# Performance work log

Measured on AMD Instinct MI355X. Metric: run time of the kernel, lower is better.

The kernel has to match this reference:

```python
import jax, jax.numpy as jnp
import numpy as np

N = 100000   # num nodes
E = 1000000  # num edges
IN = 64      # in_channels
H = 64       # hidden_dim
RESCUE_SCALE = 0.01


def setup_inputs() -> dict:
    key = jax.random.key(0)
    ks = jax.random.split(key, 8)
    x = jax.random.normal(ks[0], (N, IN), jnp.float32)
    edge_index = jax.random.randint(ks[1], (2, E), 0, N, dtype=jnp.int64)
    edge_weight = jax.random.uniform(ks[2], (E,), jnp.float32)
    glorot = lambda k, sh, fan: jax.random.normal(k, sh, jnp.float32) / np.sqrt(fan).astype(np.float32)
    W1 = glorot(ks[3], (IN, H), IN); b1 = jnp.zeros((H,), jnp.float32)
    W2 = glorot(ks[4], (H, H), H);  b2 = jnp.zeros((H,), jnp.float32)
    Wn = glorot(ks[5], (H, 1), H);  bn = jnp.zeros((1,), jnp.float32)
    Wr = glorot(ks[6], (H, 1), H);  br = jnp.zeros((1,), jnp.float32)
    return {"x": x, "edge_index": edge_index, "edge_weight": edge_weight,
            "W1": W1, "b1": b1, "W2": W2, "b2": b2,
            "Wn": Wn, "bn": bn, "Wr": Wr, "br": br}


def gcn_conv(x, src, dst, ew, W, b):
    # PyG GCNConv: linear first, then symmetric-normalized scatter-add aggregation.
    x = x @ W                                              # [N, H]
    deg = jax.ops.segment_sum(ew, dst, num_segments=N)     # weighted in-degree
    dinv = jnp.where(deg > 0, jax.lax.rsqrt(deg), 0.0)     # deg^{-1/2}, inf -> 0
    norm = dinv[src] * ew * dinv[dst]                      # [E+N]
    out = jax.ops.segment_sum(x[src] * norm[:, None], dst, num_segments=N)
    return out + b


def reference(x, edge_index, edge_weight, W1, b1, W2, b2, Wn, bn, Wr, br):
    # add self-loops with weight 1 (GCNConv default)
    loop = jnp.arange(N, dtype=edge_index.dtype)
    src = jnp.concatenate([edge_index[0], loop])
    dst = jnp.concatenate([edge_index[1], loop])
    ew = jnp.concatenate([edge_weight, jnp.ones((N,), edge_weight.dtype)])

    h = jax.nn.relu(gcn_conv(x, src, dst, ew, W1, b1))
    h = jax.nn.relu(gcn_conv(h, src, dst, ew, W2, b2))

    node_logits = (h @ Wn + bn).squeeze(-1)                # [N]
    node_selector = jax.nn.softmax(node_logits, axis=0)
    rescue_ratios = jax.nn.sigmoid((h @ Wr + br).squeeze(-1)) * RESCUE_SCALE
    return node_selector, rescue_ratios
```

## Files before the change

kernel.cpp:

```cpp
#include <hip/hip_runtime.h>
#include <hip/hip_fp16.h>
#include <math.h>

#define NN 100000
#define NE 1000000
#define CAP 32
#define OVCAP 4096
#define NEB 3907
#define NTILE 6250
#define RB 256

typedef _Float16 half8 __attribute__((ext_vector_type(8)));
typedef float f32x4 __attribute__((ext_vector_type(4)));


__global__ __launch_bounds__(256) void k_bucket(const int* __restrict__ src,
                                                const int* __restrict__ dst,
                                                const float* __restrict__ ew,
                                                int* __restrict__ cnt,
                                                int2* __restrict__ bucket,
                                                int4* __restrict__ ovf,
                                                int* __restrict__ ovf_n) {
  int e = blockIdx.x * 256 + threadIdx.x;
  if (e < NE) {
    int s = src[e];
    int d = dst[e];
    float w = ew[e];
    int pos = atomicAdd(&cnt[d], 1);
    if (pos < CAP) {
      bucket[d * CAP + pos] = make_int2(s, __float_as_int(w));
    } else {
      int t = atomicAdd(ovf_n, 1);
      if (t < OVCAP) ovf[t] = make_int4(s, d, __float_as_int(w), 0);
    }
  }
}


__device__ __forceinline__ void stage_B_lds(const float* __restrict__ W,
                                            _Float16* __restrict__ ldsB) {
  for (int u = threadIdx.x; u < 512; u += 256) {
    int slane = u & 63, ts = u >> 6;
    int t = ts >> 1, s = ts & 1;
    int qq = slane >> 4, ll = slane & 15;
#pragma unroll
    for (int j = 0; j < 8; ++j)
      ldsB[u * 8 + j] = (_Float16)W[(s * 32 + qq * 8 + j) * 64 + t * 16 + ll];
  }
}


__device__ __forceinline__ float degsum_row(const int* __restrict__ cnt,
                                            const int2* __restrict__ bucket,
                                            const int4* __restrict__ ovf,
                                            const int* __restrict__ ovf_n,
                                            int row) {
  int c = cnt[row];
  int cc = c < CAP ? c : CAP;
  float dsum = 1.0f;
  const int2* bk = bucket + (size_t)row * CAP;
  for (int j = 0; j < cc; ++j) dsum += __int_as_float(bk[j].y);
  if (c > CAP) {
    int on = ovf_n[0]; if (on > OVCAP) on = OVCAP;
    for (int t = 0; t < on; ++t) {
      int4 o = ovf[t];
      if (o.y == row) dsum += __int_as_float(o.z);
    }
  }
  return 1.0f / sqrtf(dsum);
}


__global__ __launch_bounds__(256) void k_gemm1_dinv(const float* __restrict__ X,
                                                    const float* __restrict__ W,
                                                    const int* __restrict__ cnt,
                                                    const int2* __restrict__ bucket,
                                                    const int4* __restrict__ ovf,
                                                    const int* __restrict__ ovf_n,
                                                    float* __restrict__ dinv,
                                                    __half* __restrict__ Y) {
  __shared__ _Float16 ldsB[4096];
  stage_B_lds(W, ldsB);
  __syncthreads();
  int lane = threadIdx.x & 63;
  int l15 = lane & 15, q = lane >> 4;
  half8 bfr[4][2];
#pragma unroll
  for (int t = 0; t < 4; ++t)
#pragma unroll
    for (int s = 0; s < 2; ++s)
      bfr[t][s] = *(half8*)&ldsB[((t * 2 + s) * 64 + lane) * 8];

  int wid = blockIdx.x * 4 + (threadIdx.x >> 6);
  for (int tile = wid; tile < NTILE; tile += 2048) {
    int row = tile * 16 + l15;
    float di = degsum_row(cnt, bucket, ovf, ovf_n, row);
    if (q == 0) dinv[row] = di;
    f32x4 acc[4] = {{0.f,0.f,0.f,0.f},{0.f,0.f,0.f,0.f},
                    {0.f,0.f,0.f,0.f},{0.f,0.f,0.f,0.f}};
#pragma unroll
    for (int s = 0; s < 2; ++s) {
      const float* ap = X + (size_t)row * 64 + s * 32 + q * 8;
      float4 a0 = *(const float4*)ap;
      float4 a1 = *(const float4*)(ap + 4);
      half8 af;
      af[0] = (_Float16)a0.x; af[1] = (_Float16)a0.y;
      af[2] = (_Float16)a0.z; af[3] = (_Float16)a0.w;
      af[4] = (_Float16)a1.x; af[5] = (_Float16)a1.y;
      af[6] = (_Float16)a1.z; af[7] = (_Float16)a1.w;
#pragma unroll
      for (int t = 0; t < 4; ++t)
        acc[t] = __builtin_amdgcn_mfma_f32_16x16x32_f16(af, bfr[t][s], acc[t], 0, 0, 0);
    }
#pragma unroll
    for (int r = 0; r < 4; ++r) {
      int rw = tile * 16 + q * 4 + r;
      float dv = __shfl(di, q * 4 + r, 64);
#pragma unroll
      for (int t = 0; t < 4; ++t)
        Y[(size_t)rw * 64 + t * 16 + l15] = __float2half(acc[t][r] * dv);
    }
  }
}


__device__ __forceinline__ float4 h4load(const __half* p) {
  float2 raw = *(const float2*)p;
  __half2 a = *(__half2*)&raw.x;
  __half2 b = *(__half2*)&raw.y;
  float2 fa = __half22float2(a), fb = __half22float2(b);
  return make_float4(fa.x, fa.y, fb.x, fb.y);
}

__device__ __forceinline__ float4 gather_node(const __half* __restrict__ xw,
                                              const int* __restrict__ cnt,
                                              const int2* __restrict__ bucket,
                                              const int4* __restrict__ ovf,
                                              const int* __restrict__ ovf_n,
                                              int node, int l) {
  int c = cnt[node];
  int cc = c < CAP ? c : CAP;
  const int4* bk4 = (const int4*)(bucket + (size_t)node * CAP);
  float4 acc = make_float4(0.f, 0.f, 0.f, 0.f);

  int j = 0;
  for (; j + 4 <= cc; j += 4) {
    int4 pa = bk4[j >> 1];
    int4 pb = bk4[(j >> 1) + 1];
    const float4 x0 = h4load(xw + (size_t)pa.x * 64 + l * 4);
    const float4 x1 = h4load(xw + (size_t)pa.z * 64 + l * 4);
    const float4 x2 = h4load(xw + (size_t)pb.x * 64 + l * 4);
    const float4 x3 = h4load(xw + (size_t)pb.z * 64 + l * 4);
    float v0 = __int_as_float(pa.y);
    float v1 = __int_as_float(pa.w);
    float v2 = __int_as_float(pb.y);
    float v3 = __int_as_float(pb.w);
    acc.x = fmaf(x0.x, v0, acc.x); acc.y = fmaf(x0.y, v0, acc.y);
    acc.z = fmaf(x0.z, v0, acc.z); acc.w = fmaf(x0.w, v0, acc.w);
    acc.x = fmaf(x1.x, v1, acc.x); acc.y = fmaf(x1.y, v1, acc.y);
    acc.z = fmaf(x1.z, v1, acc.z); acc.w = fmaf(x1.w, v1, acc.w);
    acc.x = fmaf(x2.x, v2, acc.x); acc.y = fmaf(x2.y, v2, acc.y);
    acc.z = fmaf(x2.z, v2, acc.z); acc.w = fmaf(x2.w, v2, acc.w);
    acc.x = fmaf(x3.x, v3, acc.x); acc.y = fmaf(x3.y, v3, acc.y);
    acc.z = fmaf(x3.z, v3, acc.z); acc.w = fmaf(x3.w, v3, acc.w);
  }
  const int2* bk = (const int2*)bk4;
  for (; j < cc; ++j) {
    int2 E = bk[j];
    const float4 xa = h4load(xw + (size_t)E.x * 64 + l * 4);
    float v = __int_as_float(E.y);
    acc.x = fmaf(xa.x, v, acc.x); acc.y = fmaf(xa.y, v, acc.y);
    acc.z = fmaf(xa.z, v, acc.z); acc.w = fmaf(xa.w, v, acc.w);
  }
  if (c > CAP) {
    int on = ovf_n[0]; if (on > OVCAP) on = OVCAP;
    for (int t = 0; t < on; ++t) {
      int4 o = ovf[t];
      if (o.y == node) {
        const float4 xa = h4load(xw + (size_t)o.x * 64 + l * 4);
        float v = __int_as_float(o.z);
        acc.x = fmaf(xa.x, v, acc.x); acc.y = fmaf(xa.y, v, acc.y);
        acc.z = fmaf(xa.z, v, acc.z); acc.w = fmaf(xa.w, v, acc.w);
      }
    }
  }
  const float4 xs = h4load(xw + (size_t)node * 64 + l * 4);
  acc.x += xs.x; acc.y += xs.y; acc.z += xs.z; acc.w += xs.w;
  return acc;
}


__global__ __launch_bounds__(256) void k_gather_gemm2(const __half* __restrict__ xw,
                                                      const float* __restrict__ dinv,
                                                      const int* __restrict__ cnt,
                                                      const int2* __restrict__ bucket,
                                                      const int4* __restrict__ ovf,
                                                      const int* __restrict__ ovf_n,
                                                      const float* __restrict__ b1,
                                                      const float* __restrict__ W2,
                                                      __half* __restrict__ Y) {
  __shared__ _Float16 ldsB[4096];
  __shared__ _Float16 ldsR[16 * 72];
  __shared__ float sdi[16];
  stage_B_lds(W2, ldsB);

  int l = threadIdx.x & 15;
  int g = threadIdx.x >> 4;
  int node = blockIdx.x * 16 + g;
  float4 acc = gather_node(xw, cnt, bucket, ovf, ovf_n, node, l);
  float di = dinv[node];
  const float4 b4 = *(const float4*)(b1 + l * 4);
  _Float16* rp = &ldsR[g * 72 + l * 4];
  rp[0] = (_Float16)fmaxf(fmaf(acc.x, di, b4.x), 0.f);
  rp[1] = (_Float16)fmaxf(fmaf(acc.y, di, b4.y), 0.f);
  rp[2] = (_Float16)fmaxf(fmaf(acc.z, di, b4.z), 0.f);
  rp[3] = (_Float16)fmaxf(fmaf(acc.w, di, b4.w), 0.f);
  if (l == 0) sdi[g] = di;
  __syncthreads();

  int lane = threadIdx.x & 63;
  int l15 = lane & 15, q = lane >> 4;
  int t = threadIdx.x >> 6;
  half8 a0 = *(half8*)&ldsR[l15 * 72 + q * 8];
  half8 a1 = *(half8*)&ldsR[l15 * 72 + 32 + q * 8];
  half8 bf0 = *(half8*)&ldsB[((t * 2 + 0) * 64 + lane) * 8];
  half8 bf1 = *(half8*)&ldsB[((t * 2 + 1) * 64 + lane) * 8];
  f32x4 acc2 = {0.f, 0.f, 0.f, 0.f};
  acc2 = __builtin_amdgcn_mfma_f32_16x16x32_f16(a0, bf0, acc2, 0, 0, 0);
  acc2 = __builtin_amdgcn_mfma_f32_16x16x32_f16(a1, bf1, acc2, 0, 0, 0);
#pragma unroll
  for (int r = 0; r < 4; ++r) {
    int rw = blockIdx.x * 16 + q * 4 + r;
    float dv = sdi[q * 4 + r];
    Y[(size_t)rw * 64 + t * 16 + l15] = __float2half(acc2[r] * dv);
  }
}


__global__ __launch_bounds__(256) void k_gather_l2_heads(const __half* __restrict__ xw2,
                                                         const float* __restrict__ dinv,
                                                         const int* __restrict__ cnt,
                                                         const int2* __restrict__ bucket,
                                                         const int4* __restrict__ ovf,
                                                         const int* __restrict__ ovf_n,
                                                         const float* __restrict__ b2,
                                                         const float* __restrict__ Wn,
                                                         const float* __restrict__ bn,
                                                         const float* __restrict__ Wr,
                                                         const float* __restrict__ br,
                                                         float* __restrict__ logits,
                                                         float* __restrict__ rr,
                                                         float* __restrict__ part) {
  __shared__ float s[256];
  int l = threadIdx.x & 15;
  int node = blockIdx.x * 16 + (threadIdx.x >> 4);
  float4 acc = gather_node(xw2, cnt, bucket, ovf, ovf_n, node, l);
  float di = dinv[node];
  const float4 b4 = *(const float4*)(b2 + l * 4);
  float4 r;
  r.x = fmaxf(fmaf(acc.x, di, b4.x), 0.f); r.y = fmaxf(fmaf(acc.y, di, b4.y), 0.f);
  r.z = fmaxf(fmaf(acc.z, di, b4.z), 0.f); r.w = fmaxf(fmaf(acc.w, di, b4.w), 0.f);
  const float4 wn4 = *(const float4*)(Wn + l * 4);
  const float4 wr4 = *(const float4*)(Wr + l * 4);
  float an = r.x * wn4.x + r.y * wn4.y + r.z * wn4.z + r.w * wn4.w;
  float ar = r.x * wr4.x + r.y * wr4.y + r.z * wr4.z + r.w * wr4.w;
#pragma unroll
  for (int m = 8; m > 0; m >>= 1) {
    an += __shfl_xor(an, m, 64);
    ar += __shfl_xor(ar, m, 64);
  }
  float lg = an + bn[0];
  if (l == 0) {
    logits[node] = lg;
    float xr = ar + br[0];
    rr[node] = 0.01f / (1.0f + expf(-xr));
  }
  s[threadIdx.x] = lg;
  __syncthreads();
  for (int w = 128; w > 0; w >>= 1) {
    if (threadIdx.x < w) s[threadIdx.x] = fmaxf(s[threadIdx.x], s[threadIdx.x + w]);
    __syncthreads();
  }
  if (threadIdx.x == 0) part[blockIdx.x] = s[0];
}


__global__ __launch_bounds__(256) void k_sexp(const float* __restrict__ logits,
                                              const float* __restrict__ part,
                                              float* __restrict__ sel,
                                              float* __restrict__ gsum) {
  __shared__ float s[256];
  float m = -INFINITY;
  for (int i = threadIdx.x; i < NTILE; i += 256) m = fmaxf(m, part[i]);
  s[threadIdx.x] = m;
  __syncthreads();
  for (int w = 128; w > 0; w >>= 1) {
    if (threadIdx.x < w) s[threadIdx.x] = fmaxf(s[threadIdx.x], s[threadIdx.x + w]);
    __syncthreads();
  }
  float gm = s[0];
  __syncthreads();
  float acc = 0.0f;
  for (int i = blockIdx.x * 256 + threadIdx.x; i < NN; i += RB * 256) {
    float e = expf(logits[i] - gm);
    sel[i] = e;
    acc += e;
  }
  s[threadIdx.x] = acc;
  __syncthreads();
  for (int w = 128; w > 0; w >>= 1) {
    if (threadIdx.x < w) s[threadIdx.x] += s[threadIdx.x + w];
    __syncthreads();
  }
  if (threadIdx.x == 0) unsafeAtomicAdd(gsum, s[0]);
}

__global__ __launch_bounds__(256) void k_snorm(float* __restrict__ sel,
                                               const float* __restrict__ gsum) {
  int i = blockIdx.x * 256 + threadIdx.x;
  if (i < NN) sel[i] *= (1.0f / gsum[0]);
}


extern "C" void kernel_launch(void* const* d_in, const int* in_sizes, int n_in,
                              void* d_out, int out_size, void* d_ws, size_t ws_size,
                              hipStream_t stream) {
  const float* x  = (const float*)d_in[0];
  const int*   ei = (const int*)d_in[1];
  const float* ew = (const float*)d_in[2];
  const float* W1 = (const float*)d_in[3];
  const float* b1 = (const float*)d_in[4];
  const float* W2 = (const float*)d_in[5];
  const float* b2 = (const float*)d_in[6];
  const float* Wn = (const float*)d_in[7];
  const float* bn = (const float*)d_in[8];
  const float* Wr = (const float*)d_in[9];
  const float* br = (const float*)d_in[10];
  const int* src = ei;
  const int* dst = ei + NE;

  char* wsb = (char*)d_ws;
  __half* xw     = (__half*)wsb;
  __half* xw2    = (__half*)(wsb + 12800000);
  float*  dinv   = (float*)(wsb + 25600000);
  float*  logits = (float*)(wsb + 26000000);
  int2*   bucket = (int2*)(wsb + 26400000);
  int4*   ovf    = (int4*)(wsb + 52000000);
  int*    cnt    = (int*)(wsb + 52065536);
  int*    ovf_n  = cnt + NN;
  float*  gsum   = (float*)(ovf_n + 1);
  float*  part1  = gsum + 1;

  float* sel = (float*)d_out;
  float* rr  = (float*)d_out + NN;

  int gN = (NN + 255) / 256;

  hipMemsetAsync(cnt, 0, (size_t)(NN + 2) * 4, stream);

  k_bucket<<<NEB, 256, 0, stream>>>(src, dst, ew, cnt, bucket, ovf, ovf_n);

  k_gemm1_dinv<<<512, 256, 0, stream>>>(x, W1, cnt, bucket, ovf, ovf_n, dinv, xw);

  k_gather_gemm2<<<NTILE, 256, 0, stream>>>(xw, dinv, cnt, bucket, ovf, ovf_n,
                                            b1, W2, xw2);

  k_gather_l2_heads<<<NTILE, 256, 0, stream>>>(xw2, dinv, cnt, bucket, ovf, ovf_n,
                                               b2, Wn, bn, Wr, br, logits, rr, part1);

  k_sexp<<<RB, 256, 0, stream>>>(logits, part1, sel, gsum);
  k_snorm<<<gN, 256, 0, stream>>>(sel, gsum);
}
```

Measured before the change: 256.0 us.

## Slice neighbor gather by source-index range for cache locality

Each node's neighbor list is now walked four times, and each pass only gathers sources whose index falls in one quarter of the node range. The aim is for concurrent waves to touch a smaller window of the feature table at a time and so hit in cache more often. In exchange, the bucket list is read four times per node, the loop has a branch per entry, and the 4-way unrolled vector bucket loads are replaced by scalar int2 loads. There is no barrier between waves, so the slices may not stay aligned across the GPU.

```diff
diff --git a/kernel.cpp b/kernel.cpp
--- a/kernel.cpp
+++ b/kernel.cpp
@@ -9,6 +9,8 @@
 #define NEB 3907
 #define NTILE 6250
 #define RB 256
+#define NSLICE 4
+#define SLICEW 25000
 
 typedef _Float16 half8 __attribute__((ext_vector_type(8)));
 typedef float f32x4 __attribute__((ext_vector_type(4)));
@@ -140,37 +142,21 @@
                                               int node, int l) {
   int c = cnt[node];
   int cc = c < CAP ? c : CAP;
-  const int4* bk4 = (const int4*)(bucket + (size_t)node * CAP);
+  const int2* bk = bucket + (size_t)node * CAP;
   float4 acc = make_float4(0.f, 0.f, 0.f, 0.f);
 
-  int j = 0;
-  for (; j + 4 <= cc; j += 4) {
-    int4 pa = bk4[j >> 1];
-    int4 pb = bk4[(j >> 1) + 1];
-    const float4 x0 = h4load(xw + (size_t)pa.x * 64 + l * 4);
-    const float4 x1 = h4load(xw + (size_t)pa.z * 64 + l * 4);
-    const float4 x2 = h4load(xw + (size_t)pb.x * 64 + l * 4);
-    const float4 x3 = h4load(xw + (size_t)pb.z * 64 + l * 4);
-    float v0 = __int_as_float(pa.y);
-    float v1 = __int_as_float(pa.w);
-    float v2 = __int_as_float(pb.y);
-    float v3 = __int_as_float(pb.w);
-    acc.x = fmaf(x0.x, v0, acc.x); acc.y = fmaf(x0.y, v0, acc.y);
-    acc.z = fmaf(x0.z, v0, acc.z); acc.w = fmaf(x0.w, v0, acc.w);
-    acc.x = fmaf(x1.x, v1, acc.x); acc.y = fmaf(x1.y, v1, acc.y);
-    acc.z = fmaf(x1.z, v1, acc.z); acc.w = fmaf(x1.w, v1, acc.w);
-    acc.x = fmaf(x2.x, v2, acc.x); acc.y = fmaf(x2.y, v2, acc.y);
-    acc.z = fmaf(x2.z, v2, acc.z); acc.w = fmaf(x2.w, v2, acc.w);
-    acc.x = fmaf(x3.x, v3, acc.x); acc.y = fmaf(x3.y, v3, acc.y);
-    acc.z = fmaf(x3.z, v3, acc.z); acc.w = fmaf(x3.w, v3, acc.w);
-  }
-  const int2* bk = (const int2*)bk4;
-  for (; j < cc; ++j) {
-    int2 E = bk[j];
-    const float4 xa = h4load(xw + (size_t)E.x * 64 + l * 4);
-    float v = __int_as_float(E.y);
-    acc.x = fmaf(xa.x, v, acc.x); acc.y = fmaf(xa.y, v, acc.y);
-    acc.z = fmaf(xa.z, v, acc.z); acc.w = fmaf(xa.w, v, acc.w);
+#pragma unroll 1
+  for (int sl = 0; sl < NSLICE; ++sl) {
+    unsigned lo = sl * SLICEW;
+    for (int j = 0; j < cc; ++j) {
+      int2 E = bk[j];
+      if ((unsigned)(E.x - lo) < (unsigned)SLICEW) {
+        const float4 xa = h4load(xw + (size_t)E.x * 64 + l * 4);
+        float v = __int_as_float(E.y);
+        acc.x = fmaf(xa.x, v, acc.x); acc.y = fmaf(xa.y, v, acc.y);
+        acc.z = fmaf(xa.z, v, acc.z); acc.w = fmaf(xa.w, v, acc.w);
+      }
+    }
   }
   if (c > CAP) {
     int on = ovf_n[0]; if (on > OVCAP) on = OVCAP;
```

New measurement: 429.4 us. 67.7% more time.
